# Kernel optimization log

Hardware: AMD Instinct MI355X
Metric: run time of the kernel (lower is better)

## Reference

```python
import jax, jax.numpy as jnp
import numpy as np

B, S, E, H = 4, 8192, 512, 8
D = E // H  # head_dim = 64


def setup_inputs() -> dict:
    key = jax.random.key(0)
    ks = jax.random.split(key, 9)
    scale = 1.0 / np.sqrt(E)
    x = jax.random.normal(ks[0], (B, S, E), dtype=jnp.float32)
    # torch nn.Linear convention: y = x @ W.T + b, W has shape (out, in)
    Wp = jax.random.uniform(ks[1], (E, E), jnp.float32, -scale, scale)
    bp = jax.random.uniform(ks[2], (E,), jnp.float32, -scale, scale)
    Wc = jax.random.uniform(ks[3], (E, E), jnp.float32, -scale, scale)
    bc = jax.random.uniform(ks[4], (E,), jnp.float32, -scale, scale)
    Ws = jax.random.uniform(ks[5], (E, E), jnp.float32, -scale, scale)
    bs = jax.random.uniform(ks[6], (E,), jnp.float32, -scale, scale)
    Wo = jax.random.uniform(ks[7], (E, E), jnp.float32, -scale, scale)
    bo = jax.random.uniform(ks[8], (E,), jnp.float32, -scale, scale)
    return {"x": x, "Wp": Wp, "bp": bp, "Wc": Wc, "bc": bc,
            "Ws": Ws, "bs": bs, "Wo": Wo, "bo": bo}


def reference(x, Wp, bp, Wc, bc, Ws, bs, Wo, bo):
    # Faithful to TreeAttention.forward with tree_structure=None (default path).
    # NOTE: original views projections as (B,S,H,D) without transposing head/seq,
    # so the matmuls mix HEADS per token (HxH scores), not tokens.
    b, s, _ = x.shape
    parent = (jnp.einsum('bse,fe->bsf', x, Wp) + bp).reshape(b, s, H, D)
    child = (jnp.einsum('bse,fe->bsf', x, Wc) + bc).reshape(b, s, H, D)
    sibling = (jnp.einsum('bse,fe->bsf', x, Ws) + bs).reshape(b, s, H, D)
    # per-token head-mixing scores: (B, S, H, H)
    scores = jnp.einsum('bshd,bstd->bsht', parent, child) / jnp.sqrt(
        jnp.asarray(D, dtype=x.dtype))
    attention = jax.nn.softmax(scores, axis=-1)
    # dropout is identity in eval mode (reference runs in inference mode)
    out = jnp.einsum('bsht,bstd->bshd', attention, sibling).reshape(b, s, E)
    return jnp.einsum('bse,fe->bsf', out, Wo) + bo
```

## Files before the change

### kernel.cpp

```cpp
#include <hip/hip_runtime.h>
#include <hip/hip_bf16.h>

typedef unsigned short u16;
typedef __attribute__((ext_vector_type(8))) short bf16x8;
typedef __attribute__((ext_vector_type(4))) float f32x4;
typedef __attribute__((ext_vector_type(8))) unsigned short u16x8;

#define GLDS(gp, lp) __builtin_amdgcn_global_load_lds( \
    (const __attribute__((address_space(1))) void*)(gp), \
    (__attribute__((address_space(3))) void*)(lp), 16, 0, 0)

__device__ __forceinline__ u16 f2b(float f) {
  unsigned u = __builtin_bit_cast(unsigned, f);
  return (u16)((u + 0x7fffu + ((u >> 16) & 1u)) >> 16);
}
__device__ __forceinline__ float b2f(u16 s) {
  return __builtin_bit_cast(float, (unsigned)s << 16);
}

__global__ __launch_bounds__(256) void convert_k(
    const float* __restrict__ x, const float* __restrict__ Wp,
    const float* __restrict__ Wc, const float* __restrict__ Ws,
    const float* __restrict__ Wo, u16* __restrict__ xb,
    u16* __restrict__ wall, u16* __restrict__ wob)
{
  const long CX = 2097152;
  const long CW = 98304;
  const long CO = 32768;
  const long total = CX + CW + CO;
  for (long i = (long)blockIdx.x * blockDim.x + threadIdx.x; i < total;
       i += (long)gridDim.x * blockDim.x) {
    const float* src; u16* dst;
    if (i < CX) {
      src = x + i * 8; dst = xb + i * 8;
    } else if (i < CX + CW) {
      long e = (i - CX) * 8;
      int n = (int)(e >> 9), k = (int)(e & 511);
      const float* wr = (n < 512)  ? (Wp + (long)n * 512)
                      : (n < 1024) ? (Wc + (long)(n - 512) * 512)
                                   : (Ws + (long)(n - 1024) * 512);
      src = wr + k; dst = wall + e;
    } else {
      long e = (i - CX - CW) * 8; src = Wo + e; dst = wob + e;
    }
    f32x4 v0 = *(const f32x4*)src;
    f32x4 v1 = *(const f32x4*)(src + 4);
    u16x8 o;
    o[0]=f2b(v0[0]); o[1]=f2b(v0[1]); o[2]=f2b(v0[2]); o[3]=f2b(v0[3]);
    o[4]=f2b(v1[0]); o[5]=f2b(v1[1]); o[6]=f2b(v1[2]); o[7]=f2b(v1[3]);
    *(u16x8*)dst = o;
  }
}

template<int NC, bool BF16OUT>
__global__ __launch_bounds__(256) void gemm_bt(
    const u16* __restrict__ A, const u16* __restrict__ Bw,
    const float* __restrict__ bias0, const float* __restrict__ bias1,
    const float* __restrict__ bias2, void* __restrict__ Cout)
{
  __shared__ alignas(16) u16 lA[128 * 32];
  __shared__ alignas(16) u16 lB[128 * 32];
  const int tid = threadIdx.x;
  const int w = tid >> 6, lane = tid & 63;
  const int wr = w >> 1, wc = w & 1;
  const long row0 = (long)blockIdx.y * 128;
  const int col0 = blockIdx.x * 128;

  const int ob = w * 1024 + (lane << 4);
  const int rA = ob >> 6;
  const int kb = (ob & 63) >> 1;
  const u16* gA0 = A + (row0 + rA) * 512 + kb;
  const u16* gA1 = gA0 + 64 * 512;
  const u16* gB0 = Bw + ((long)(col0 + rA)) * 512 + kb;
  const u16* gB1 = gB0 + 64 * 512;
  char* lAc = (char*)lA; char* lBc = (char*)lB;
  char* dA0 = lAc + w * 1024; char* dA1 = lAc + 4096 + w * 1024;
  char* dB0 = lBc + w * 1024; char* dB1 = lBc + 4096 + w * 1024;

  const u16* fA = lA + (wr * 64 + (lane & 15)) * 32 + ((lane >> 4) << 3);
  const u16* fB = lB + (wc * 64 + (lane & 15)) * 32 + ((lane >> 4) << 3);

  f32x4 acc[4][4] = {};
  for (int kt = 0; kt < 16; ++kt) {
    const int ko = kt * 32;
    __syncthreads();
    GLDS(gA0 + ko, dA0); GLDS(gA1 + ko, dA1);
    GLDS(gB0 + ko, dB0); GLDS(gB1 + ko, dB1);
    __syncthreads();
    bf16x8 aF[4], bF[4];
#pragma unroll
    for (int m = 0; m < 4; ++m) aF[m] = *(const bf16x8*)(fA + m * 16 * 32);
#pragma unroll
    for (int n = 0; n < 4; ++n) bF[n] = *(const bf16x8*)(fB + n * 16 * 32);
#pragma unroll
    for (int m = 0; m < 4; ++m)
#pragma unroll
      for (int n = 0; n < 4; ++n)
        acc[m][n] = __builtin_amdgcn_mfma_f32_16x16x32_bf16(aF[m], bF[n], acc[m][n], 0, 0, 0);
  }

  const int colB = col0 + wc * 64 + (lane & 15);
  const long rowB = row0 + wr * 64 + ((lane >> 4) << 2);
#pragma unroll
  for (int n = 0; n < 4; ++n) {
    const int col = colB + n * 16;
    const float* bptr = (NC == 512) ? bias0
                        : (col < 512 ? bias0 : (col < 1024 ? bias1 : bias2));
    const float bv = bptr[col & 511];
#pragma unroll
    for (int m = 0; m < 4; ++m)
#pragma unroll
      for (int j = 0; j < 4; ++j) {
        const long row = rowB + m * 16 + j;
        const float v = acc[m][n][j] + bv;
        if (BF16OUT) ((u16*)Cout)[row * NC + col] = f2b(v);
        else         ((float*)Cout)[row * NC + col] = v;
      }
  }
}

__global__ __launch_bounds__(256) void attn_k(const u16* __restrict__ PCS,
                                              u16* __restrict__ OUT)
{
  __shared__ float L[4][1664];
  const int w = threadIdx.x >> 6, lane = threadIdx.x & 63;
  const long token = (long)blockIdx.x * 4 + w;
  float* Lw = L[w];
  const int C0 = 544, S0 = 1088, AT0 = 1600;
  const u16* rowp = PCS + token * 1536;
#pragma unroll
  for (int q = 0; q < 3; ++q) {
    u16x8 v = *(const u16x8*)(rowp + q * 512 + lane * 8);
    float* dst = (q < 2) ? (Lw + q * 544 + (lane >> 3) * 68 + (lane & 7) * 8)
                         : (Lw + S0 + lane * 8);
    f32x4 a = {b2f(v[0]), b2f(v[1]), b2f(v[2]), b2f(v[3])};
    f32x4 b = {b2f(v[4]), b2f(v[5]), b2f(v[6]), b2f(v[7])};
    *(f32x4*)dst = a;
    *(f32x4*)(dst + 4) = b;
  }
  const int h = lane >> 3, t = lane & 7;
  float sc = 0.f;
#pragma unroll
  for (int d = 0; d < 64; d += 4) {
    f32x4 pv = *(const f32x4*)(Lw + h * 68 + d);
    f32x4 cv = *(const f32x4*)(Lw + C0 + t * 68 + d);
    sc += pv[0]*cv[0] + pv[1]*cv[1] + pv[2]*cv[2] + pv[3]*cv[3];
  }
  sc *= 0.125f;
  float mx = sc;
  mx = fmaxf(mx, __shfl_xor(mx, 1));
  mx = fmaxf(mx, __shfl_xor(mx, 2));
  mx = fmaxf(mx, __shfl_xor(mx, 4));
  float e = __expf(sc - mx);
  float sm = e;
  sm += __shfl_xor(sm, 1);
  sm += __shfl_xor(sm, 2);
  sm += __shfl_xor(sm, 4);
  Lw[AT0 + lane] = e / sm;
  float o[8] = {0, 0, 0, 0, 0, 0, 0, 0};
#pragma unroll
  for (int tt = 0; tt < 8; ++tt) {
    const float av = Lw[AT0 + h * 8 + tt];
    f32x4 s0 = *(const f32x4*)(Lw + S0 + tt * 64 + t * 8);
    f32x4 s1 = *(const f32x4*)(Lw + S0 + tt * 64 + t * 8 + 4);
    o[0] += av * s0[0]; o[1] += av * s0[1]; o[2] += av * s0[2]; o[3] += av * s0[3];
    o[4] += av * s1[0]; o[5] += av * s1[1]; o[6] += av * s1[2]; o[7] += av * s1[3];
  }
  u16x8 ov;
#pragma unroll
  for (int j = 0; j < 8; ++j) ov[j] = f2b(o[j]);
  *(u16x8*)(OUT + token * 512 + lane * 8) = ov;
}

extern "C" void kernel_launch(void* const* d_in, const int* in_sizes, int n_in,
                              void* d_out, int out_size, void* d_ws, size_t ws_size,
                              hipStream_t stream) {
  const float* x  = (const float*)d_in[0];
  const float* Wp = (const float*)d_in[1];
  const float* bp = (const float*)d_in[2];
  const float* Wc = (const float*)d_in[3];
  const float* bc = (const float*)d_in[4];
  const float* Ws = (const float*)d_in[5];
  const float* bs = (const float*)d_in[6];
  const float* Wo = (const float*)d_in[7];
  const float* bo = (const float*)d_in[8];

  char* ws = (char*)d_ws;
  u16* xb   = (u16*)ws;
  u16* wall = (u16*)(ws + 33554432);
  u16* wob  = (u16*)(ws + 35127296);
  u16* pcs  = (u16*)(ws + 35651584);
  u16* outb = xb;

  convert_k<<<2048, 256, 0, stream>>>(x, Wp, Wc, Ws, Wo, xb, wall, wob);
  gemm_bt<1536, true><<<dim3(12, 256), 256, 0, stream>>>(xb, wall, bp, bc, bs, pcs);
  attn_k<<<8192, 256, 0, stream>>>(pcs, outb);
  gemm_bt<512, false><<<dim3(4, 256), 256, 0, stream>>>(outb, wob, bo, bo, bo, d_out);
}
```

Before: 163.5 us.

## Replace GEMM with 256x256 double-buffered 8-wave kernel using swizzled LDS

Measured after the change: 154.6 us. 5.4% less time.

```diff
diff --git a/kernel.cpp b/kernel.cpp
--- a/kernel.cpp
+++ b/kernel.cpp
@@ -17,6 +17,10 @@
 __device__ __forceinline__ float b2f(u16 s) {
   return __builtin_bit_cast(float, (unsigned)s << 16);
 }
+
+#define BARX() do { __builtin_amdgcn_sched_barrier(0); \
+  asm volatile("s_barrier" ::: "memory"); \
+  __builtin_amdgcn_sched_barrier(0); } while (0)
 
 __global__ __launch_bounds__(256) void convert_k(
     const float* __restrict__ x, const float* __restrict__ Wp,
@@ -53,70 +57,122 @@
 }
 
 template<int NC, bool BF16OUT>
-__global__ __launch_bounds__(256) void gemm_bt(
+__global__ __launch_bounds__(512, 2) void gemm8(
     const u16* __restrict__ A, const u16* __restrict__ Bw,
     const float* __restrict__ bias0, const float* __restrict__ bias1,
     const float* __restrict__ bias2, void* __restrict__ Cout)
 {
-  __shared__ alignas(16) u16 lA[128 * 32];
-  __shared__ alignas(16) u16 lB[128 * 32];
+  __shared__ alignas(16) u16 sA[2][16384];
+  __shared__ alignas(16) u16 sB[2][16384];
+  char* sAc = (char*)sA;
+  char* sBc = (char*)sB;
+
   const int tid = threadIdx.x;
   const int w = tid >> 6, lane = tid & 63;
-  const int wr = w >> 1, wc = w & 1;
-  const long row0 = (long)blockIdx.y * 128;
-  const int col0 = blockIdx.x * 128;
-
-  const int ob = w * 1024 + (lane << 4);
-  const int rA = ob >> 6;
-  const int kb = (ob & 63) >> 1;
-  const u16* gA0 = A + (row0 + rA) * 512 + kb;
-  const u16* gA1 = gA0 + 64 * 512;
-  const u16* gB0 = Bw + ((long)(col0 + rA)) * 512 + kb;
-  const u16* gB1 = gB0 + 64 * 512;
-  char* lAc = (char*)lA; char* lBc = (char*)lB;
-  char* dA0 = lAc + w * 1024; char* dA1 = lAc + 4096 + w * 1024;
-  char* dB0 = lBc + w * 1024; char* dB1 = lBc + 4096 + w * 1024;
-
-  const u16* fA = lA + (wr * 64 + (lane & 15)) * 32 + ((lane >> 4) << 3);
-  const u16* fB = lB + (wc * 64 + (lane & 15)) * 32 + ((lane >> 4) << 3);
-
-  f32x4 acc[4][4] = {};
-  for (int kt = 0; kt < 16; ++kt) {
-    const int ko = kt * 32;
-    __syncthreads();
-    GLDS(gA0 + ko, dA0); GLDS(gA1 + ko, dA1);
-    GLDS(gB0 + ko, dB0); GLDS(gB1 + ko, dB1);
-    __syncthreads();
-    bf16x8 aF[4], bF[4];
-#pragma unroll
-    for (int m = 0; m < 4; ++m) aF[m] = *(const bf16x8*)(fA + m * 16 * 32);
-#pragma unroll
-    for (int n = 0; n < 4; ++n) bF[n] = *(const bf16x8*)(fB + n * 16 * 32);
-#pragma unroll
-    for (int m = 0; m < 4; ++m)
-#pragma unroll
-      for (int n = 0; n < 4; ++n)
-        acc[m][n] = __builtin_amdgcn_mfma_f32_16x16x32_bf16(aF[m], bF[n], acc[m][n], 0, 0, 0);
-  }
-
-  const int colB = col0 + wc * 64 + (lane & 15);
-  const long rowB = row0 + wr * 64 + ((lane >> 4) << 2);
+  const int wr = w >> 2, wc = w & 3;
+  const int ln15 = lane & 15, g4 = lane >> 4, l7 = lane & 7;
+
+  const int nbx = NC / 256;
+  const int nwg = nbx * 128;
+  const int qq = nwg / 8;
+  const int flat = blockIdx.x;
+  const int swz = (flat & 7) * qq + (flat >> 3);
+  const int bx = swz % nbx, by = swz / nbx;
+  const long row0 = (long)by * 256;
+  const int col0 = bx * 256;
+
+  const int gsw = (tid & 7) ^ ((tid >> 3) & 7);
+  const u16* pA = A + (row0 + (tid >> 3)) * 512 + gsw * 8;
+  const u16* pB = Bw + ((long)col0 + (tid >> 3)) * 512 + gsw * 8;
+
+#define STAGE(pp, tt) do { \
+    const u16* a0_ = pA + (tt) * 64; const u16* b0_ = pB + (tt) * 64; \
+    char* da_ = sAc + (pp) * 32768 + w * 1024; \
+    char* db_ = sBc + (pp) * 32768 + w * 1024; \
+    GLDS(a0_, da_);          GLDS(a0_ + 32768, da_ + 8192); \
+    GLDS(a0_ + 65536, da_ + 16384); GLDS(a0_ + 98304, da_ + 24576); \
+    GLDS(b0_, db_);          GLDS(b0_ + 32768, db_ + 8192); \
+    GLDS(b0_ + 65536, db_ + 16384); GLDS(b0_ + 98304, db_ + 24576); \
+  } while (0)
+
+  const int gkb0 = ((0 + g4) ^ l7) * 16;
+  const int gkb1 = ((4 + g4) ^ l7) * 16;
+  const int arow = (wr * 128 + ln15) * 128;
+  const int brow = (wc * 64 + ln15) * 128;
+
+#define LOAD_A(MH) do { \
+    _Pragma("unroll") for (int mf = 0; mf < 4; ++mf) { \
+      aF[mf][0] = *(const bf16x8*)(bufA + (MH) * 8192 + mf * 2048 + gkb0); \
+      aF[mf][1] = *(const bf16x8*)(bufA + (MH) * 8192 + mf * 2048 + gkb1); \
+    } } while (0)
+#define LOAD_B(NH, BF) do { \
+    _Pragma("unroll") for (int nf = 0; nf < 2; ++nf) { \
+      BF[nf][0] = *(const bf16x8*)(bufB + (NH) * 4096 + nf * 2048 + gkb0); \
+      BF[nf][1] = *(const bf16x8*)(bufB + (NH) * 4096 + nf * 2048 + gkb1); \
+    } } while (0)
+#define MFMA_Q(MH, NH, BF) do { \
+    _Pragma("unroll") for (int mf = 0; mf < 4; ++mf) \
+    _Pragma("unroll") for (int nf = 0; nf < 2; ++nf) { \
+      f32x4 c_ = acc[(MH) * 4 + mf][(NH) * 2 + nf]; \
+      c_ = __builtin_amdgcn_mfma_f32_16x16x32_bf16(aF[mf][0], BF[nf][0], c_, 0, 0, 0); \
+      c_ = __builtin_amdgcn_mfma_f32_16x16x32_bf16(aF[mf][1], BF[nf][1], c_, 0, 0, 0); \
+      acc[(MH) * 4 + mf][(NH) * 2 + nf] = c_; \
+    } } while (0)
+
+  f32x4 acc[8][4] = {};
+
+  STAGE(0, 0);
+  asm volatile("s_waitcnt vmcnt(0)" ::: "memory");
+  BARX();
+
+  for (int t = 0; t < 8; ++t) {
+    const int p = t & 1;
+    const char* bufA = sAc + p * 32768 + arow;
+    const char* bufB = sBc + p * 32768 + brow;
+    bf16x8 aF[4][2], bFa[2][2], bFb[2][2];
+
+    LOAD_A(0); LOAD_B(0, bFa);
+    if (t < 7) STAGE(p ^ 1, t + 1);
+    BARX();
+    __builtin_amdgcn_s_setprio(1); MFMA_Q(0, 0, bFa); __builtin_amdgcn_s_setprio(0);
+    BARX();
+    LOAD_B(1, bFb);
+    BARX();
+    __builtin_amdgcn_s_setprio(1); MFMA_Q(0, 1, bFb); __builtin_amdgcn_s_setprio(0);
+    BARX();
+    LOAD_A(1);
+    BARX();
+    __builtin_amdgcn_s_setprio(1); MFMA_Q(1, 1, bFb); __builtin_amdgcn_s_setprio(0);
+    BARX();
+    __builtin_amdgcn_s_setprio(1); MFMA_Q(1, 0, bFa); __builtin_amdgcn_s_setprio(0);
+    if (t < 7) {
+      asm volatile("s_waitcnt vmcnt(0)" ::: "memory");
+      BARX();
+    }
+  }
+
+  const long rowE = row0 + wr * 128 + (g4 << 2);
+  const int colE = col0 + wc * 64 + ln15;
 #pragma unroll
   for (int n = 0; n < 4; ++n) {
-    const int col = colB + n * 16;
+    const int col = colE + n * 16;
     const float* bptr = (NC == 512) ? bias0
                         : (col < 512 ? bias0 : (col < 1024 ? bias1 : bias2));
     const float bv = bptr[col & 511];
 #pragma unroll
-    for (int m = 0; m < 4; ++m)
+    for (int mi = 0; mi < 8; ++mi)
 #pragma unroll
       for (int j = 0; j < 4; ++j) {
-        const long row = rowB + m * 16 + j;
-        const float v = acc[m][n][j] + bv;
+        const long row = rowE + mi * 16 + j;
+        const float v = acc[mi][n][j] + bv;
         if (BF16OUT) ((u16*)Cout)[row * NC + col] = f2b(v);
         else         ((float*)Cout)[row * NC + col] = v;
       }
   }
+#undef STAGE
+#undef LOAD_A
+#undef LOAD_B
+#undef MFMA_Q
 }
 
 __global__ __launch_bounds__(256) void attn_k(const u16* __restrict__ PCS,
@@ -193,7 +249,7 @@
   u16* outb = xb;
 
   convert_k<<<2048, 256, 0, stream>>>(x, Wp, Wc, Ws, Wo, xb, wall, wob);
-  gemm_bt<1536, true><<<dim3(12, 256), 256, 0, stream>>>(xb, wall, bp, bc, bs, pcs);
+  gemm8<1536, true><<<768, 512, 0, stream>>>(xb, wall, bp, bc, bs, pcs);
   attn_k<<<8192, 256, 0, stream>>>(pcs, outb);
-  gemm_bt<512, false><<<dim3(4, 256), 256, 0, stream>>>(outb, wob, bo, bo, bo, d_out);
-}
+  gemm8<512, false><<<256, 512, 0, stream>>>(outb, wob, bo, bo, bo, d_out);
+}
```
